# Performance work log

Hardware: AMD Instinct MI355X
Metric: run time of the kernel (lower is better)

Reference implementation:

```python
import jax, jax.numpy as jnp
import numpy as np

B, S, H, DEPTH = 2, 2048, 8, 64
D_MODEL = H * DEPTH  # 512


def setup_inputs() -> dict:
    key = jax.random.key(0)
    ks = jax.random.split(key, 6)
    s = 0.02
    return {
        "emb_x": jax.random.normal(ks[0], (B, S, D_MODEL), dtype=jnp.float32),
        "pe_rel_t": jax.random.normal(ks[1], (B, S, D_MODEL), dtype=jnp.float32),
        "Wq": jax.random.normal(ks[2], (D_MODEL, D_MODEL), dtype=jnp.float32) * s,
        "bq": jnp.zeros((D_MODEL,), dtype=jnp.float32),
        "Wk": jax.random.normal(ks[3], (D_MODEL, D_MODEL), dtype=jnp.float32) * s,
        "bk": jnp.zeros((D_MODEL,), dtype=jnp.float32),
        "Wv": jax.random.normal(ks[4], (D_MODEL, D_MODEL), dtype=jnp.float32) * s,
        "bv": jnp.zeros((D_MODEL,), dtype=jnp.float32),
        "Wo": jax.random.normal(ks[5], (D_MODEL, D_MODEL), dtype=jnp.float32) * s,
        "bo": jnp.zeros((D_MODEL,), dtype=jnp.float32),
    }


def _split_heads(x):
    # [B, S, D_MODEL] -> [B, H, S, DEPTH]
    b, s, _ = x.shape
    return x.reshape(b, s, H, DEPTH).transpose(0, 2, 1, 3)


def reference(emb_x, pe_rel_t, Wq, bq, Wk, bk, Wv, bv, Wo, bo):
    # RPE attention: content and relative-position streams share WQ/WK.
    Q_c = _split_heads(emb_x @ Wq + bq)
    Q_r = _split_heads(pe_rel_t @ Wq + bq)
    K_c = _split_heads(emb_x @ Wk + bk)
    K_r = _split_heads(pe_rel_t @ Wk + bk)
    V_c = _split_heads(emb_x @ Wv + bv)

    logits = (
        jnp.einsum("bhqd,bhkd->bhqk", Q_c, K_c)
        + jnp.einsum("bhqd,bhkd->bhqk", Q_r, K_c)
        + jnp.einsum("bhqd,bhkd->bhqk", Q_c, K_r)
    ) / jnp.sqrt(jnp.asarray(DEPTH, dtype=emb_x.dtype))

    attn = jax.nn.softmax(logits, axis=-1)  # [B, H, S, S]
    z = jnp.einsum("bhqk,bhkd->bhqd", attn, V_c)  # [B, H, S, DEPTH]
    z = z.transpose(0, 2, 1, 3).reshape(emb_x.shape[0], -1, D_MODEL)
    out = z @ Wo + bo
    return out, attn
```

## Files before the change

### kernel.cpp

```cpp
#include <hip/hip_runtime.h>
#include <hip/hip_bf16.h>


typedef __bf16 bf16;
typedef bf16 bf16x4 __attribute__((ext_vector_type(4)));
typedef bf16 bf16x8 __attribute__((ext_vector_type(8)));
typedef float f32x4 __attribute__((ext_vector_type(4)));

#define B_ 2
#define S_ 2048
#define H_ 8
#define D_ 64
#define DM_ 512
#define M_ 4096

__global__ __launch_bounds__(256) void pack_x(const float4* __restrict__ emb,
                                              const float4* __restrict__ pe,
                                              bf16* __restrict__ xb,
                                              bf16* __restrict__ xp,
                                              bf16* __restrict__ xs) {
    int i = blockIdx.x * 256 + threadIdx.x;
    float4 a = emb[i], b = pe[i];
    int o = i * 4;
    bf16x4 va, vp, vs;
    va.x = (bf16)a.x; va.y = (bf16)a.y; va.z = (bf16)a.z; va.w = (bf16)a.w;
    vp.x = (bf16)b.x; vp.y = (bf16)b.y; vp.z = (bf16)b.z; vp.w = (bf16)b.w;
    vs.x = (bf16)(a.x + b.x); vs.y = (bf16)(a.y + b.y);
    vs.z = (bf16)(a.z + b.z); vs.w = (bf16)(a.w + b.w);
    *(bf16x4*)(xb + o) = va;
    *(bf16x4*)(xp + o) = vp;
    *(bf16x4*)(xs + o) = vs;
}

__global__ __launch_bounds__(256) void pack_w4(const float* __restrict__ Wq,
                                               const float* __restrict__ Wk,
                                               const float* __restrict__ Wv,
                                               const float* __restrict__ Wo,
                                               bf16* __restrict__ WT) {
    __shared__ float t[32][33];
    const float* W = (blockIdx.z == 0) ? Wq : (blockIdx.z == 1) ? Wk
                   : (blockIdx.z == 2) ? Wv : Wo;
    bf16* dst = WT + (long)blockIdx.z * (DM_ * DM_);
    const int r = threadIdx.x >> 5, c = threadIdx.x & 31;
    const int kb = blockIdx.x * 32, nb = blockIdx.y * 32;
    for (int i = 0; i < 4; ++i)
        t[r + 8 * i][c] = W[(long)(kb + r + 8 * i) * 512 + nb + c];
    __syncthreads();
    for (int i = 0; i < 4; ++i)
        dst[(long)(nb + r + 8 * i) * 512 + kb + c] = (bf16)t[c][r + 8 * i];
}

__global__ __launch_bounds__(256) void proj_fused(
    const bf16* __restrict__ Xb, const bf16* __restrict__ Xp,
    const bf16* __restrict__ Xs, const bf16* __restrict__ WT,
    const float* __restrict__ bq, const float* __restrict__ bk,
    const float* __restrict__ bv,
    bf16* __restrict__ Qc, bf16* __restrict__ Qr, bf16* __restrict__ Kc,
    bf16* __restrict__ Ks, bf16* __restrict__ Vt) {
    __shared__ bf16 As[64][72];
    __shared__ bf16 Bs[64][72];

    const int z = blockIdx.z;
    const bf16* A = (z == 1) ? Xp : (z == 3) ? Xs : Xb;
    const bf16* BT = WT + (long)(z >> 1) * (DM_ * DM_);
    const float* bias = (z >= 4) ? bv : (z >= 2) ? bk : bq;
    const float bscale = (z == 3) ? 2.f : 1.f;
    bf16* dst = (z == 0) ? Qc : (z == 1) ? Qr : (z == 2) ? Kc
              : (z == 3) ? Ks : Vt;
    const bool vmode = (z == 4);

    const int tid = threadIdx.x;
    const int lane = tid & 63;
    const int wave = tid >> 6;
    const int wm = wave >> 1, wn = wave & 1;
    const int row0 = blockIdx.x * 64;
    const int col0 = blockIdx.y * 64;
    const int lm = lane & 15, lk = (lane >> 4) * 8;
    const int r0 = tid >> 3, sg0 = (tid & 7) * 8;

    f32x4 acc[2][2] = {{{0.f,0.f,0.f,0.f},{0.f,0.f,0.f,0.f}},
                       {{0.f,0.f,0.f,0.f},{0.f,0.f,0.f,0.f}}};

    bf16x8 ra[2], rb[2];
    auto load_ab = [&](int k0) {
        ra[0] = *(const bf16x8*)(A + (long)(row0 + r0) * 512 + k0 + sg0);
        ra[1] = *(const bf16x8*)(A + (long)(row0 + r0 + 32) * 512 + k0 + sg0);
        rb[0] = *(const bf16x8*)(BT + (long)(col0 + r0) * 512 + k0 + sg0);
        rb[1] = *(const bf16x8*)(BT + (long)(col0 + r0 + 32) * 512 + k0 + sg0);
    };

    load_ab(0);
    for (int k0 = 0; k0 < 512; k0 += 64) {
        *(bf16x8*)&As[r0][sg0]      = ra[0];
        *(bf16x8*)&As[r0 + 32][sg0] = ra[1];
        *(bf16x8*)&Bs[r0][sg0]      = rb[0];
        *(bf16x8*)&Bs[r0 + 32][sg0] = rb[1];
        __syncthreads();
        if (k0 < 448) load_ab(k0 + 64);
        for (int kk = 0; kk < 64; kk += 32) {
            bf16x8 af[2], bfr[2];
            for (int t = 0; t < 2; ++t) {
                af[t]  = *(const bf16x8*)&As[wm * 32 + t * 16 + lm][kk + lk];
                bfr[t] = *(const bf16x8*)&Bs[wn * 32 + t * 16 + lm][kk + lk];
            }
            for (int mt = 0; mt < 2; ++mt)
                for (int nt = 0; nt < 2; ++nt)
                    acc[mt][nt] = __builtin_amdgcn_mfma_f32_16x16x32_bf16(
                        af[mt], bfr[nt], acc[mt][nt], 0, 0, 0);
        }
        __syncthreads();
    }

    const int rbase = (lane >> 4) * 4;
    for (int mt = 0; mt < 2; ++mt)
        for (int nt = 0; nt < 2; ++nt)
            for (int r = 0; r < 4; ++r) {
                int row = row0 + wm * 32 + mt * 16 + rbase + r;
                int col = col0 + wn * 32 + nt * 16 + lm;
                float v = acc[mt][nt][r] + bias[col] * bscale;
                int b = row >> 11, s = row & 2047, h = col >> 6, d = col & 63;
                if (!vmode)
                    dst[(((long)(b * H_ + h) * S_ + s) * 64) + d] = (bf16)v;
                else
                    dst[(((long)(b * H_ + h) * 64 + d) * S_) + s] = (bf16)v;
            }
}

__global__ __launch_bounds__(256) void proj_out(const bf16* __restrict__ Zb,
                                                const bf16* __restrict__ WoT,
                                                const float* __restrict__ bo,
                                                float* __restrict__ Out) {
    __shared__ bf16 As[64][72];
    __shared__ bf16 Bs[64][72];
    const int tid = threadIdx.x;
    const int lane = tid & 63;
    const int wave = tid >> 6;
    const int wm = wave >> 1, wn = wave & 1;
    const int row0 = blockIdx.x * 64;
    const int col0 = blockIdx.y * 64;
    const int lm = lane & 15, lk = (lane >> 4) * 8;
    const int r0 = tid >> 3, sg0 = (tid & 7) * 8;

    f32x4 acc[2][2] = {{{0.f,0.f,0.f,0.f},{0.f,0.f,0.f,0.f}},
                       {{0.f,0.f,0.f,0.f},{0.f,0.f,0.f,0.f}}};

    bf16x8 ra[2], rb[2];
    auto load_ab = [&](int k0) {
        const int acol = k0 + sg0;
        const int h = acol >> 6, d = acol & 63;
        {
            int arow = row0 + r0;
            int b = arow >> 11, s = arow & 2047;
            ra[0] = *(const bf16x8*)(Zb + (((long)(b * H_ + h) * S_ + s) * 64) + d);
        }
        {
            int arow = row0 + r0 + 32;
            int b = arow >> 11, s = arow & 2047;
            ra[1] = *(const bf16x8*)(Zb + (((long)(b * H_ + h) * S_ + s) * 64) + d);
        }
        rb[0] = *(const bf16x8*)(WoT + (long)(col0 + r0) * 512 + k0 + sg0);
        rb[1] = *(const bf16x8*)(WoT + (long)(col0 + r0 + 32) * 512 + k0 + sg0);
    };

    load_ab(0);
    for (int k0 = 0; k0 < 512; k0 += 64) {
        *(bf16x8*)&As[r0][sg0]      = ra[0];
        *(bf16x8*)&As[r0 + 32][sg0] = ra[1];
        *(bf16x8*)&Bs[r0][sg0]      = rb[0];
        *(bf16x8*)&Bs[r0 + 32][sg0] = rb[1];
        __syncthreads();
        if (k0 < 448) load_ab(k0 + 64);
        for (int kk = 0; kk < 64; kk += 32) {
            bf16x8 af[2], bfr[2];
            for (int t = 0; t < 2; ++t) {
                af[t]  = *(const bf16x8*)&As[wm * 32 + t * 16 + lm][kk + lk];
                bfr[t] = *(const bf16x8*)&Bs[wn * 32 + t * 16 + lm][kk + lk];
            }
            for (int mt = 0; mt < 2; ++mt)
                for (int nt = 0; nt < 2; ++nt)
                    acc[mt][nt] = __builtin_amdgcn_mfma_f32_16x16x32_bf16(
                        af[mt], bfr[nt], acc[mt][nt], 0, 0, 0);
        }
        __syncthreads();
    }

    const int rbase = (lane >> 4) * 4;
    for (int mt = 0; mt < 2; ++mt)
        for (int nt = 0; nt < 2; ++nt)
            for (int r = 0; r < 4; ++r) {
                int row = row0 + wm * 32 + mt * 16 + rbase + r;
                int col = col0 + wn * 32 + nt * 16 + lm;
                Out[(long)row * 512 + col] = acc[mt][nt][r] + bo[col];
            }
}

__global__ __launch_bounds__(256) void attn_kernel(const bf16* __restrict__ Qc,
                                                   const bf16* __restrict__ Qr,
                                                   const bf16* __restrict__ Kc,
                                                   const bf16* __restrict__ Ks,
                                                   const bf16* __restrict__ Vt,
                                                   bf16* __restrict__ Zb,
                                                   float* __restrict__ attn_out) {
    __shared__ bf16 Kcs[64][72];
    __shared__ bf16 Kss[64][72];
    __shared__ bf16 Vts[64][72];
    __shared__ bf16 ptile[4][16][40];

    const int tid = threadIdx.x, lane = tid & 63, wave = tid >> 6;
    const int bh = blockIdx.x >> 5;
    const int qt = blockIdx.x & 31;
    const int qw = qt * 64 + wave * 16;
    const long kbase = (long)bh * (S_ * 64);
    const long vbase = (long)bh * (64 * S_);
    const int lm = lane & 15, lk = (lane >> 4) * 8;
    const int r0 = tid >> 3, sg0 = (tid & 7) * 8;
    const float SC = 0.125f;

    bf16x8 qcf[2], qrf[2];
    for (int kt = 0; kt < 2; ++kt) {
        long off = kbase + (long)(qw + lm) * 64 + kt * 32 + lk;
        qcf[kt] = *(const bf16x8*)(Qc + off);
        qrf[kt] = *(const bf16x8*)(Qr + off);
    }

    float rsum[4] = {0.f, 0.f, 0.f, 0.f};
    f32x4 zacc[4] = {{0.f,0.f,0.f,0.f},{0.f,0.f,0.f,0.f},
                     {0.f,0.f,0.f,0.f},{0.f,0.f,0.f,0.f}};

    bf16x8 rk[2], rs[2], rv[2];
    auto load_kv = [&](int key0) {
        rk[0] = *(const bf16x8*)(Kc + kbase + (long)(key0 + r0) * 64 + sg0);
        rk[1] = *(const bf16x8*)(Kc + kbase + (long)(key0 + r0 + 32) * 64 + sg0);
        rs[0] = *(const bf16x8*)(Ks + kbase + (long)(key0 + r0) * 64 + sg0);
        rs[1] = *(const bf16x8*)(Ks + kbase + (long)(key0 + r0 + 32) * 64 + sg0);
        rv[0] = *(const bf16x8*)(Vt + vbase + (long)r0 * S_ + key0 + sg0);
        rv[1] = *(const bf16x8*)(Vt + vbase + (long)(r0 + 32) * S_ + key0 + sg0);
    };

    load_kv(0);
    for (int key0 = 0; key0 < S_; key0 += 64) {
        __syncthreads();
        *(bf16x8*)&Kcs[r0][sg0]      = rk[0];
        *(bf16x8*)&Kcs[r0 + 32][sg0] = rk[1];
        *(bf16x8*)&Kss[r0][sg0]      = rs[0];
        *(bf16x8*)&Kss[r0 + 32][sg0] = rs[1];
        *(bf16x8*)&Vts[r0][sg0]      = rv[0];
        *(bf16x8*)&Vts[r0 + 32][sg0] = rv[1];
        __syncthreads();
        if (key0 + 64 < S_) load_kv(key0 + 64);

        for (int pair = 0; pair < 2; ++pair) {
            for (int nt = 0; nt < 2; ++nt) {
                const int keyl = pair * 32 + nt * 16;
                f32x4 acc = {0.f, 0.f, 0.f, 0.f};
                for (int kt = 0; kt < 2; ++kt) {
                    bf16x8 bs = *(const bf16x8*)&Kss[keyl + lm][kt * 32 + lk];
                    bf16x8 bc = *(const bf16x8*)&Kcs[keyl + lm][kt * 32 + lk];
                    acc = __builtin_amdgcn_mfma_f32_16x16x32_bf16(qcf[kt], bs, acc, 0, 0, 0);
                    acc = __builtin_amdgcn_mfma_f32_16x16x32_bf16(qrf[kt], bc, acc, 0, 0, 0);
                }
                for (int r = 0; r < 4; ++r) {
                    float p = __expf(acc[r] * SC);
                    rsum[r] += p;
                    ptile[wave][(lane >> 4) * 4 + r][nt * 16 + lm] = (bf16)p;
                }
            }
            bf16x8 pa = *(const bf16x8*)&ptile[wave][lm][lk];
            for (int nt = 0; nt < 4; ++nt) {
                bf16x8 vb = *(const bf16x8*)&Vts[nt * 16 + lm][pair * 32 + lk];
                zacc[nt] = __builtin_amdgcn_mfma_f32_16x16x32_bf16(pa, vb, zacc[nt], 0, 0, 0);
            }
        }
    }

    float inv_r[4];
    for (int r = 0; r < 4; ++r) {
        float s = rsum[r];
        s += __shfl_xor(s, 1);
        s += __shfl_xor(s, 2);
        s += __shfl_xor(s, 4);
        s += __shfl_xor(s, 8);
        inv_r[r] = 1.0f / s;
    }

    auto load_k = [&](int key0) {
        rk[0] = *(const bf16x8*)(Kc + kbase + (long)(key0 + r0) * 64 + sg0);
        rk[1] = *(const bf16x8*)(Kc + kbase + (long)(key0 + r0 + 32) * 64 + sg0);
        rs[0] = *(const bf16x8*)(Ks + kbase + (long)(key0 + r0) * 64 + sg0);
        rs[1] = *(const bf16x8*)(Ks + kbase + (long)(key0 + r0 + 32) * 64 + sg0);
    };
    load_k(0);

    for (int nt = 0; nt < 4; ++nt)
        for (int r = 0; r < 4; ++r)
            Zb[kbase + (long)(qw + (lane >> 4) * 4 + r) * 64 + nt * 16 + lm] =
                (bf16)(zacc[nt][r] * inv_r[r]);

    const long abase = (long)bh * S_ * S_;
    for (int key0 = 0; key0 < S_; key0 += 64) {
        __syncthreads();
        *(bf16x8*)&Kcs[r0][sg0]      = rk[0];
        *(bf16x8*)&Kcs[r0 + 32][sg0] = rk[1];
        *(bf16x8*)&Kss[r0][sg0]      = rs[0];
        *(bf16x8*)&Kss[r0 + 32][sg0] = rs[1];
        __syncthreads();
        if (key0 + 64 < S_) load_k(key0 + 64);

        for (int nt = 0; nt < 4; ++nt) {
            const int keyl = nt * 16;
            f32x4 acc = {0.f, 0.f, 0.f, 0.f};
            for (int kt = 0; kt < 2; ++kt) {
                bf16x8 bs = *(const bf16x8*)&Kss[keyl + lm][kt * 32 + lk];
                bf16x8 bc = *(const bf16x8*)&Kcs[keyl + lm][kt * 32 + lk];
                acc = __builtin_amdgcn_mfma_f32_16x16x32_bf16(qcf[kt], bs, acc, 0, 0, 0);
                acc = __builtin_amdgcn_mfma_f32_16x16x32_bf16(qrf[kt], bc, acc, 0, 0, 0);
            }
            for (int r = 0; r < 4; ++r) {
                float p = __expf(acc[r] * SC) * inv_r[r];
                attn_out[abase + (long)(qw + (lane >> 4) * 4 + r) * S_ + key0 + keyl + lm] = p;
            }
        }
    }
}

extern "C" void kernel_launch(void* const* d_in, const int* in_sizes, int n_in,
                              void* d_out, int out_size, void* d_ws, size_t ws_size,
                              hipStream_t stream) {
    const float* emb = (const float*)d_in[0];
    const float* pe  = (const float*)d_in[1];
    const float* Wq  = (const float*)d_in[2];
    const float* bq  = (const float*)d_in[3];
    const float* Wk  = (const float*)d_in[4];
    const float* bk  = (const float*)d_in[5];
    const float* Wv  = (const float*)d_in[6];
    const float* bv  = (const float*)d_in[7];
    const float* Wo  = (const float*)d_in[8];
    const float* bo  = (const float*)d_in[9];

    float* outp = (float*)d_out;
    float* attn = outp + (long)B_ * S_ * DM_;

    char* w = (char*)d_ws;
    const long SZ_X = (long)M_ * DM_ * 2;
    const long SZ_W = (long)DM_ * DM_ * 2;
    bf16* Xb  = (bf16*)(w);
    bf16* Xp  = (bf16*)(w + SZ_X);
    bf16* Xs  = (bf16*)(w + 2 * SZ_X);
    bf16* WqT = (bf16*)(w + 3 * SZ_X);
    bf16* WoT = (bf16*)(w + 3 * SZ_X + 3 * SZ_W);
    char* p2  = w + 3 * SZ_X + 4 * SZ_W;
    bf16* Qc  = (bf16*)(p2);
    bf16* Qr  = (bf16*)(p2 + SZ_X);
    bf16* Kc  = (bf16*)(p2 + 2 * SZ_X);
    bf16* Ks  = (bf16*)(p2 + 3 * SZ_X);
    bf16* Vt  = (bf16*)(p2 + 4 * SZ_X);
    bf16* Zb  = (bf16*)(p2 + 5 * SZ_X);

    pack_x<<<(M_ * DM_ / 4) / 256, 256, 0, stream>>>(
        (const float4*)emb, (const float4*)pe, Xb, Xp, Xs);
    pack_w4<<<dim3(16, 16, 4), 256, 0, stream>>>(Wq, Wk, Wv, Wo, WqT);

    proj_fused<<<dim3(M_ / 64, DM_ / 64, 5), 256, 0, stream>>>(
        Xb, Xp, Xs, WqT, bq, bk, bv, Qc, Qr, Kc, Ks, Vt);

    attn_kernel<<<B_ * H_ * (S_ / 64), 256, 0, stream>>>(
        Qc, Qr, Kc, Ks, Vt, Zb, attn);

    proj_out<<<dim3(M_ / 64, DM_ / 64), 256, 0, stream>>>(Zb, WoT, bo, outp);
}
```

Before: 420.3 us.

## Split attention into key-split forward and parallel probability-write kernels

The single attention kernel is split in two. The first uses 512-thread blocks where two wave groups process interleaved key tiles and merge their partial Z and row sums through LDS, then writes Z and the inverse row sums. The second kernel recomputes logits over a grid that also splits the key dimension into four chunks, and writes the normalized probabilities as 16-byte nontemporal row-contiguous stores using swapped MFMA operands. This is meant to raise parallelism and store efficiency for the large attention output, at the cost of an extra launch and a small invR buffer.

```diff
diff --git a/kernel.cpp b/kernel.cpp
--- a/kernel.cpp
+++ b/kernel.cpp
@@ -194,26 +194,29 @@
             }
 }
 
-__global__ __launch_bounds__(256) void attn_kernel(const bf16* __restrict__ Qc,
+__global__ __launch_bounds__(512, 4) void attn_fwd(const bf16* __restrict__ Qc,
                                                    const bf16* __restrict__ Qr,
                                                    const bf16* __restrict__ Kc,
                                                    const bf16* __restrict__ Ks,
                                                    const bf16* __restrict__ Vt,
                                                    bf16* __restrict__ Zb,
-                                                   float* __restrict__ attn_out) {
-    __shared__ bf16 Kcs[64][72];
-    __shared__ bf16 Kss[64][72];
-    __shared__ bf16 Vts[64][72];
-    __shared__ bf16 ptile[4][16][40];
+                                                   float* __restrict__ invR) {
+    __shared__ bf16 Kcs[2][64][72];
+    __shared__ bf16 Kss[2][64][72];
+    __shared__ bf16 Vts[2][64][72];
+    __shared__ bf16 ptile[8][16][40];
+    __shared__ float rsLds[4][16];
 
     const int tid = threadIdx.x, lane = tid & 63, wave = tid >> 6;
+    const int grp = wave >> 2, w4 = wave & 3;
     const int bh = blockIdx.x >> 5;
     const int qt = blockIdx.x & 31;
-    const int qw = qt * 64 + wave * 16;
+    const int qw = qt * 64 + w4 * 16;
     const long kbase = (long)bh * (S_ * 64);
     const long vbase = (long)bh * (64 * S_);
     const int lm = lane & 15, lk = (lane >> 4) * 8;
-    const int r0 = tid >> 3, sg0 = (tid & 7) * 8;
+    const int gtid = tid & 255;
+    const int r0 = gtid >> 3, sg0 = (gtid & 7) * 8;
     const float SC = 0.125f;
 
     bf16x8 qcf[2], qrf[2];
@@ -237,25 +240,25 @@
         rv[1] = *(const bf16x8*)(Vt + vbase + (long)(r0 + 32) * S_ + key0 + sg0);
     };
 
-    load_kv(0);
-    for (int key0 = 0; key0 < S_; key0 += 64) {
-        __syncthreads();
-        *(bf16x8*)&Kcs[r0][sg0]      = rk[0];
-        *(bf16x8*)&Kcs[r0 + 32][sg0] = rk[1];
-        *(bf16x8*)&Kss[r0][sg0]      = rs[0];
-        *(bf16x8*)&Kss[r0 + 32][sg0] = rs[1];
-        *(bf16x8*)&Vts[r0][sg0]      = rv[0];
-        *(bf16x8*)&Vts[r0 + 32][sg0] = rv[1];
-        __syncthreads();
-        if (key0 + 64 < S_) load_kv(key0 + 64);
+    load_kv(grp * 64);
+    for (int t = grp; t < 32; t += 2) {
+        __syncthreads();
+        *(bf16x8*)&Kcs[grp][r0][sg0]      = rk[0];
+        *(bf16x8*)&Kcs[grp][r0 + 32][sg0] = rk[1];
+        *(bf16x8*)&Kss[grp][r0][sg0]      = rs[0];
+        *(bf16x8*)&Kss[grp][r0 + 32][sg0] = rs[1];
+        *(bf16x8*)&Vts[grp][r0][sg0]      = rv[0];
+        *(bf16x8*)&Vts[grp][r0 + 32][sg0] = rv[1];
+        __syncthreads();
+        if (t + 2 < 32) load_kv((t + 2) * 64);
 
         for (int pair = 0; pair < 2; ++pair) {
             for (int nt = 0; nt < 2; ++nt) {
                 const int keyl = pair * 32 + nt * 16;
                 f32x4 acc = {0.f, 0.f, 0.f, 0.f};
                 for (int kt = 0; kt < 2; ++kt) {
-                    bf16x8 bs = *(const bf16x8*)&Kss[keyl + lm][kt * 32 + lk];
-                    bf16x8 bc = *(const bf16x8*)&Kcs[keyl + lm][kt * 32 + lk];
+                    bf16x8 bs = *(const bf16x8*)&Kss[grp][keyl + lm][kt * 32 + lk];
+                    bf16x8 bc = *(const bf16x8*)&Kcs[grp][keyl + lm][kt * 32 + lk];
                     acc = __builtin_amdgcn_mfma_f32_16x16x32_bf16(qcf[kt], bs, acc, 0, 0, 0);
                     acc = __builtin_amdgcn_mfma_f32_16x16x32_bf16(qrf[kt], bc, acc, 0, 0, 0);
                 }
@@ -267,44 +270,96 @@
             }
             bf16x8 pa = *(const bf16x8*)&ptile[wave][lm][lk];
             for (int nt = 0; nt < 4; ++nt) {
-                bf16x8 vb = *(const bf16x8*)&Vts[nt * 16 + lm][pair * 32 + lk];
+                bf16x8 vb = *(const bf16x8*)&Vts[grp][nt * 16 + lm][pair * 32 + lk];
                 zacc[nt] = __builtin_amdgcn_mfma_f32_16x16x32_bf16(pa, vb, zacc[nt], 0, 0, 0);
             }
         }
     }
 
-    float inv_r[4];
     for (int r = 0; r < 4; ++r) {
         float s = rsum[r];
         s += __shfl_xor(s, 1);
         s += __shfl_xor(s, 2);
         s += __shfl_xor(s, 4);
         s += __shfl_xor(s, 8);
-        inv_r[r] = 1.0f / s;
-    }
-
+        rsum[r] = s;
+    }
+
+    __syncthreads();
+    float* zp = (float*)&Kcs[0][0][0];
+    const int qlb = (lane >> 4) * 4;
+    if (grp == 1) {
+        for (int nt = 0; nt < 4; ++nt)
+            for (int r = 0; r < 4; ++r)
+                zp[(w4 * 16 + qlb + r) * 68 + nt * 16 + lm] = zacc[nt][r];
+        if (lm == 0)
+            for (int r = 0; r < 4; ++r) rsLds[w4][qlb + r] = rsum[r];
+    }
+    __syncthreads();
+    if (grp == 0) {
+        float inv_r[4];
+        for (int r = 0; r < 4; ++r)
+            inv_r[r] = 1.0f / (rsum[r] + rsLds[w4][qlb + r]);
+        for (int nt = 0; nt < 4; ++nt)
+            for (int r = 0; r < 4; ++r) {
+                float zv = zacc[nt][r] + zp[(w4 * 16 + qlb + r) * 68 + nt * 16 + lm];
+                Zb[kbase + (long)(qw + qlb + r) * 64 + nt * 16 + lm] =
+                    (bf16)(zv * inv_r[r]);
+            }
+        if (lm == 0)
+            for (int r = 0; r < 4; ++r)
+                invR[bh * S_ + qw + qlb + r] = inv_r[r];
+    }
+}
+
+__global__ __launch_bounds__(256) void attn_wr(const bf16* __restrict__ Qc,
+                                               const bf16* __restrict__ Qr,
+                                               const bf16* __restrict__ Kc,
+                                               const bf16* __restrict__ Ks,
+                                               const float* __restrict__ invR,
+                                               float* __restrict__ attn_out) {
+    __shared__ bf16 Kcs[64][72];
+    __shared__ bf16 Kss[64][72];
+
+    const int tid = threadIdx.x, lane = tid & 63, wave = tid >> 6;
+    const int bh = blockIdx.z;
+    const int qt = blockIdx.x;
+    const int kc = blockIdx.y;
+    const int qw = qt * 64 + wave * 16;
+    const long kbase = (long)bh * (S_ * 64);
+    const long abase = (long)bh * S_ * S_;
+    const int lm = lane & 15, lk = (lane >> 4) * 8;
+    const int kg = lane >> 4;
+    const int r0 = tid >> 3, sg0 = (tid & 7) * 8;
+    const float SC = 0.125f;
+
+    bf16x8 qcf[2], qrf[2];
+    for (int kt = 0; kt < 2; ++kt) {
+        long off = kbase + (long)(qw + lm) * 64 + kt * 32 + lk;
+        qcf[kt] = *(const bf16x8*)(Qc + off);
+        qrf[kt] = *(const bf16x8*)(Qr + off);
+    }
+    const float invq = invR[bh * S_ + qw + lm];
+    const long qrow = abase + (long)(qw + lm) * S_;
+
+    bf16x8 rk[2], rs[2];
     auto load_k = [&](int key0) {
         rk[0] = *(const bf16x8*)(Kc + kbase + (long)(key0 + r0) * 64 + sg0);
         rk[1] = *(const bf16x8*)(Kc + kbase + (long)(key0 + r0 + 32) * 64 + sg0);
         rs[0] = *(const bf16x8*)(Ks + kbase + (long)(key0 + r0) * 64 + sg0);
         rs[1] = *(const bf16x8*)(Ks + kbase + (long)(key0 + r0 + 32) * 64 + sg0);
     };
-    load_k(0);
-
-    for (int nt = 0; nt < 4; ++nt)
-        for (int r = 0; r < 4; ++r)
-            Zb[kbase + (long)(qw + (lane >> 4) * 4 + r) * 64 + nt * 16 + lm] =
-                (bf16)(zacc[nt][r] * inv_r[r]);
-
-    const long abase = (long)bh * S_ * S_;
-    for (int key0 = 0; key0 < S_; key0 += 64) {
+
+    load_k(kc * 512);
+    for (int t = 0; t < 8; ++t) {
+        const int key0 = kc * 512 + t * 64;
         __syncthreads();
         *(bf16x8*)&Kcs[r0][sg0]      = rk[0];
         *(bf16x8*)&Kcs[r0 + 32][sg0] = rk[1];
         *(bf16x8*)&Kss[r0][sg0]      = rs[0];
         *(bf16x8*)&Kss[r0 + 32][sg0] = rs[1];
         __syncthreads();
-        if (key0 + 64 < S_) load_k(key0 + 64);
+        if (t < 7) load_k(key0 + 64);
 
         for (int nt = 0; nt < 4; ++nt) {
             const int keyl = nt * 16;
@@ -312,13 +367,13 @@
             for (int kt = 0; kt < 2; ++kt) {
                 bf16x8 bs = *(const bf16x8*)&Kss[keyl + lm][kt * 32 + lk];
                 bf16x8 bc = *(const bf16x8*)&Kcs[keyl + lm][kt * 32 + lk];
-                acc = __builtin_amdgcn_mfma_f32_16x16x32_bf16(qcf[kt], bs, acc, 0, 0, 0);
-                acc = __builtin_amdgcn_mfma_f32_16x16x32_bf16(qrf[kt], bc, acc, 0, 0, 0);
-            }
-            for (int r = 0; r < 4; ++r) {
-                float p = __expf(acc[r] * SC) * inv_r[r];
-                attn_out[abase + (long)(qw + (lane >> 4) * 4 + r) * S_ + key0 + keyl + lm] = p;
-            }
+                acc = __builtin_amdgcn_mfma_f32_16x16x32_bf16(bs, qcf[kt], acc, 0, 0, 0);
+                acc = __builtin_amdgcn_mfma_f32_16x16x32_bf16(bc, qrf[kt], acc, 0, 0, 0);
+            }
+            f32x4 p;
+            for (int r = 0; r < 4; ++r) p[r] = __expf(acc[r] * SC) * invq;
+            f32x4* dst = (f32x4*)(attn_out + qrow + key0 + keyl + kg * 4);
+            __builtin_nontemporal_store(p, dst);
         }
     }
 }
@@ -355,6 +410,7 @@
     bf16* Ks  = (bf16*)(p2 + 3 * SZ_X);
     bf16* Vt  = (bf16*)(p2 + 4 * SZ_X);
     bf16* Zb  = (bf16*)(p2 + 5 * SZ_X);
+    float* invR = (float*)(p2 + 6 * SZ_X);
 
     pack_x<<<(M_ * DM_ / 4) / 256, 256, 0, stream>>>(
         (const float4*)emb, (const float4*)pe, Xb, Xp, Xs);
@@ -363,8 +419,11 @@
     proj_fused<<<dim3(M_ / 64, DM_ / 64, 5), 256, 0, stream>>>(
         Xb, Xp, Xs, WqT, bq, bk, bv, Qc, Qr, Kc, Ks, Vt);
 
-    attn_kernel<<<B_ * H_ * (S_ / 64), 256, 0, stream>>>(
-        Qc, Qr, Kc, Ks, Vt, Zb, attn);
+    attn_fwd<<<B_ * H_ * (S_ / 64), 512, 0, stream>>>(
+        Qc, Qr, Kc, Ks, Vt, Zb, invR);
+
+    attn_wr<<<dim3(S_ / 64, 4, B_ * H_), 256, 0, stream>>>(
+        Qc, Qr, Kc, Ks, invR, attn);
 
     proj_out<<<dim3(M_ / 64, DM_ / 64), 256, 0, stream>>>(Zb, WoT, bo, outp);
 }
```

Measured after the change: 427.3 us. No clear change (+1.7%).
